# Optimization experiments

Measured on AMD Instinct MI355X. Metric: run time of the kernel, lower is better.

Reference implementation:

```python
import jax, jax.numpy as jnp
import numpy as np

NOT_EPSILON = 1.0
B, Q, K, T = 2, 512, 512, 256  # batch, num queries, num keys, dims


def swishmax(x, axis):
    # x * exp(x - max) / (sum(|x * exp(x - max)|) + 1)
    xexp = x * jnp.exp(x - jnp.max(x, axis=axis, keepdims=True))
    return xexp / (jnp.sum(jnp.abs(xexp), axis=axis, keepdims=True) + NOT_EPSILON)


def setup_inputs() -> dict:
    key = jax.random.key(0)
    ks = jax.random.split(key, 8)
    s = 1.0 / np.sqrt(T)
    return {
        "query_tokens": jax.random.normal(ks[0], (B, Q, T), jnp.float32),
        "key_tokens": jax.random.normal(ks[1], (B, K, T), jnp.float32),
        "value_tokens": jax.random.normal(ks[2], (B, K, T), jnp.float32),
        "Wk": jax.random.normal(ks[3], (T, T), jnp.float32) * s,
        "Wq": jax.random.normal(ks[4], (T, T), jnp.float32) * s,
        "Wva": jax.random.normal(ks[5], (T, T), jnp.float32) * s,
        "Wal": jax.random.normal(ks[6], (T, T), jnp.float32) * s,
        "Wvo": jax.random.normal(ks[7], (T, T), jnp.float32) * s,
    }


def reference(query_tokens, key_tokens, value_tokens, Wk, Wq, Wva, Wal, Wvo):
    # torch nn.Linear: y = x @ W.T (no biases)
    k = jnp.einsum('bkt,ut->bku', key_tokens, Wk)      # [B,K,T]
    q = jnp.einsum('bqt,ut->bqu', query_tokens, Wq)    # [B,Q,T]
    # elementwise outer product over token pairs: [B,K,Q,T]
    raw = k[:, :, None, :] * q[:, None, :, :]
    logits = jnp.einsum('bkqt,ut->bkqu', raw, Wal)     # [B,K,Q,T]
    scale = swishmax(logits, axis=-2)                  # normalize over Q
    v = jnp.einsum('bkt,ut->bku', value_tokens, Wva)   # [B,K,T]
    values_scaled = v[:, :, None, :] * scale           # [B,K,Q,T]
    value_sum = values_scaled.sum(axis=-3)             # sum over K -> [B,Q,T]
    return jnp.einsum('bqt,ut->bqu', value_sum, Wvo)   # [B,Q,T]
```

## Files before the change

### kernel.cpp

```cpp
#include <hip/hip_runtime.h>
#include <cstdint>


typedef short bf16x8 __attribute__((ext_vector_type(8)));
typedef float f32x4  __attribute__((ext_vector_type(4)));

__device__ inline float bf2f(short s) {
  return __uint_as_float(((unsigned)(unsigned short)s) << 16);
}
__device__ inline unsigned packrn(float lo, float hi) {
  return __builtin_amdgcn_perm(__float_as_uint(hi) + 0x8000u,
                               __float_as_uint(lo) + 0x8000u, 0x07060302u);
}
__device__ inline unsigned encM(float f) {
  unsigned k = (unsigned)__float_as_int(f);
  return (k & 0x80000000u) ? ~k : (k | 0x80000000u);
}
__device__ inline float decM(unsigned k) {
  int i = (k & 0x80000000u) ? (int)(k ^ 0x80000000u) : (int)~k;
  return __int_as_float(i);
}

#define FMA16()                                                                 \
  c[0][0] += a.x*w.x; c[0][1] += a.x*w.y; c[0][2] += a.x*w.z; c[0][3] += a.x*w.w; \
  c[1][0] += a.y*w.x; c[1][1] += a.y*w.y; c[1][2] += a.y*w.z; c[1][3] += a.y*w.w; \
  c[2][0] += a.z*w.x; c[2][1] += a.z*w.y; c[2][2] += a.z*w.z; c[2][3] += a.z*w.w; \
  c[3][0] += a.w*w.x; c[3][1] += a.w*w.y; c[3][2] += a.w*w.z; c[3][3] += a.w*w.w;

#define GEMM_BODY_RM(X, W)                                                      \
  __shared__ __align__(16) float As[16][68];                                    \
  __shared__ __align__(16) float Ws[16][68];                                    \
  const int tid = threadIdx.x;                                                  \
  const int tx4 = (tid & 15) * 4;                                               \
  const int ty4 = (tid >> 4) * 4;                                               \
  const int m0 = blockIdx.x * 64, u0 = blockIdx.y * 64;                         \
  const int lmi = tid >> 2, lc4 = (tid & 3) * 4;                                \
  float c[4][4] = {};                                                           \
  _Pragma("unroll 1")                                                           \
  for (int t0 = 0; t0 < 256; t0 += 16) {                                        \
    const float4 xa = *(const float4*)&(X)[(size_t)(m0 + lmi) * 256 + t0 + lc4];\
    const float4 wb = *(const float4*)&(W)[(size_t)(u0 + lmi) * 256 + t0 + lc4];\
    __syncthreads();                                                            \
    As[lc4 + 0][lmi] = xa.x; As[lc4 + 1][lmi] = xa.y;                           \
    As[lc4 + 2][lmi] = xa.z; As[lc4 + 3][lmi] = xa.w;                           \
    Ws[lc4 + 0][lmi] = wb.x; Ws[lc4 + 1][lmi] = wb.y;                           \
    Ws[lc4 + 2][lmi] = wb.z; Ws[lc4 + 3][lmi] = wb.w;                           \
    __syncthreads();                                                            \
    _Pragma("unroll")                                                           \
    for (int t = 0; t < 16; ++t) {                                              \
      const float4 a = *(const float4*)&As[t][ty4];                             \
      const float4 w = *(const float4*)&Ws[t][tx4];                             \
      FMA16();                                                                  \
    }                                                                           \
  }

__global__ __launch_bounds__(256) void proj3(
    const float* __restrict__ key, const float* __restrict__ value,
    const float* __restrict__ query, const float* __restrict__ Wk,
    const float* __restrict__ Wq, const float* __restrict__ Wva,
    const float* __restrict__ Wal, float* __restrict__ kproj,
    float* __restrict__ vproj, short* __restrict__ qpF,
    short* __restrict__ WalF, float* __restrict__ vsum)
{
  const int z = blockIdx.z;
  if (z == 3) {
    const int p = blockIdx.x * 4 + blockIdx.y;
    const int t256 = threadIdx.x;
#pragma unroll
    for (int e = 0; e < 4; ++e) {
      const int d = p * 1024 + t256 * 4 + e;
      const int j = d & 7, uu = (d >> 3) & 31, c8g = d >> 8;
      const int ucx = c8g >> 5, cc = c8g & 31;
      const float v = Wal[(ucx * 32 + uu) * 256 + cc * 8 + j];
      WalF[d] = (short)packrn(v, v);
    }
    float4* vz = (float4*)(vsum + p * 4096);
#pragma unroll
    for (int e = 0; e < 4; ++e) vz[t256 * 4 + e] = make_float4(0.f, 0.f, 0.f, 0.f);
    return;
  }
  const float* X = (z == 0) ? key : (z == 1) ? value : query;
  const float* W = (z == 0) ? Wk  : (z == 1) ? Wva   : Wq;
  GEMM_BODY_RM(X, W);
  if (z == 2) {
    const int tbase = u0 + tx4;
    const int ks = tbase >> 5, l4f = (tbase & 31) >> 3, j0 = tbase & 7;
#pragma unroll
    for (int i = 0; i < 4; ++i) {
      const int m = m0 + ty4 + i;
      const int bb = m >> 9, q = m & 511;
      const int g = q >> 4, l15q = q & 15;
      const size_t idx = ((size_t)(((bb * 32 + g) * 8 + ks) * 64) + l4f * 16 + l15q) * 8 + j0;
      uint2 s; s.x = packrn(c[i][0], c[i][1]); s.y = packrn(c[i][2], c[i][3]);
      *(uint2*)&qpF[idx] = s;
    }
  } else {
    float* C = (z == 0) ? kproj : vproj;
#pragma unroll
    for (int i = 0; i < 4; ++i)
      *(float4*)&C[(size_t)(m0 + ty4 + i) * 256 + u0 + tx4] =
          make_float4(c[i][0], c[i][1], c[i][2], c[i][3]);
  }
}

__global__ __launch_bounds__(256) void gemm_out(
    const float* __restrict__ X, const float* __restrict__ W, float* __restrict__ out)
{
  GEMM_BODY_RM(X, W);
#pragma unroll
  for (int i = 0; i < 4; ++i)
    *(float4*)&out[(size_t)(m0 + ty4 + i) * 256 + u0 + tx4] =
        make_float4(c[i][0], c[i][1], c[i][2], c[i][3]);
}

union Frag { bf16x8 v; unsigned u[4]; };

__global__ __launch_bounds__(1024, 4) void kernelC(
    const short* __restrict__ qpF, const float* __restrict__ kproj,
    const float* __restrict__ vproj, const short* __restrict__ WalF,
    float* __restrict__ vsum)
{
  __shared__ __align__(16) short W2F[2][8192];
  __shared__ float vpS[32 * 33];
  __shared__ unsigned statM[96];
  __shared__ float statS[96];

  const int kt = blockIdx.x, uc = blockIdx.y, b = blockIdx.z;
  const int u0 = uc * 32, k0 = kt * 32;
  const int tid = threadIdx.x;
  const int lane = tid & 63, w = tid >> 6;
  const int l15 = lane & 15, l4 = lane >> 4;
  const int uu = tid & 31, c8 = tid >> 5;

  if (tid < 96) { statM[tid] = 0u; statS[tid] = 0.f; }
  vpS[c8 * 33 + uu] = vproj[(size_t)(b * 512 + k0 + c8) * 256 + u0 + uu];

  float wl[8];
  {
    const bf16x8 w0 = *(const bf16x8*)&WalF[((size_t)(uc * 32 + c8) * 32 + uu) * 8];
#pragma unroll
    for (int j = 0; j < 8; ++j) wl[j] = bf2f(w0[j]);
  }

  const short* qbase = qpF + (size_t)b * 131072;
  Frag qa[2][8];
#pragma unroll
  for (int qg = 0; qg < 2; ++qg)
#pragma unroll
    for (int ks = 0; ks < 8; ++ks) {
      qa[qg][ks].v = *(const bf16x8*)&qbase[(((size_t)(w * 2 + qg) * 8 + ks) * 64 + lane) * 8];
      asm volatile("" : "+v"(qa[qg][ks].u[0]), "+v"(qa[qg][ks].u[1]),
                        "+v"(qa[qg][ks].u[2]), "+v"(qa[qg][ks].u[3]));
    }

  {
    const long krow = (long)(b * 512 + k0) * 256;
    const f32x4 a0 = *(const f32x4*)&kproj[krow + c8 * 8];
    const f32x4 a1 = *(const f32x4*)&kproj[krow + c8 * 8 + 4];
    uint4 st;
    st.x = packrn(wl[0] * a0[0], wl[1] * a0[1]);
    st.y = packrn(wl[2] * a0[2], wl[3] * a0[3]);
    st.z = packrn(wl[4] * a1[0], wl[5] * a1[1]);
    st.w = packrn(wl[6] * a1[2], wl[7] * a1[3]);
    *(uint4*)&W2F[0][(c8 * 32 + uu) * 8] = st;
  }
  __syncthreads();

  const f32x4 z4 = {0.f, 0.f, 0.f, 0.f};
  f32x4 acc[2][2] = {z4, z4, z4, z4};

#pragma unroll 1
  for (int kk = 0; kk < 32; ++kk) {
    const int cs = kk & 1, ss = kk % 3;

    f32x4 a0, a1;
    if (kk < 31) {
      const long krn = (long)(b * 512 + k0 + kk + 1) * 256;
      a0 = *(const f32x4*)&kproj[krn + c8 * 8];
      a1 = *(const f32x4*)&kproj[krn + c8 * 8 + 4];
    }

    f32x4 lg[2][2] = {z4, z4, z4, z4};
#pragma unroll
    for (int ks = 0; ks < 8; ++ks) {
      const bf16x8 f0 = *(const bf16x8*)&W2F[cs][((ks * 4 + l4) * 32 + l15) * 8];
      const bf16x8 f1 = *(const bf16x8*)&W2F[cs][((ks * 4 + l4) * 32 + 16 + l15) * 8];
#pragma unroll
      for (int qg = 0; qg < 2; ++qg) {
        lg[qg][0] = __builtin_amdgcn_mfma_f32_16x16x32_bf16(qa[qg][ks].v, f0, lg[qg][0], 0, 0, 0);
        lg[qg][1] = __builtin_amdgcn_mfma_f32_16x16x32_bf16(qa[qg][ks].v, f1, lg[qg][1], 0, 0, 0);
      }
    }

    if (kk < 31) {
      uint4 st;
      st.x = packrn(wl[0] * a0[0], wl[1] * a0[1]);
      st.y = packrn(wl[2] * a0[2], wl[3] * a0[3]);
      st.z = packrn(wl[4] * a1[0], wl[5] * a1[1]);
      st.w = packrn(wl[6] * a1[2], wl[7] * a1[3]);
      *(uint4*)&W2F[cs ^ 1][(c8 * 32 + uu) * 8] = st;
    }

    float Mv[2], Sv[2];
#pragma unroll
    for (int ug = 0; ug < 2; ++ug) {
      float m = lg[0][ug][0];
#pragma unroll
      for (int qg = 0; qg < 2; ++qg)
#pragma unroll
        for (int i = 0; i < 4; ++i) m = fmaxf(m, lg[qg][ug][i]);
      float s = 0.f;
#pragma unroll
      for (int qg = 0; qg < 2; ++qg)
#pragma unroll
        for (int i = 0; i < 4; ++i) {
          const float x = lg[qg][ug][i];
          const float p = x * __expf(x);
          lg[qg][ug][i] = p;
          s += fabsf(p);
        }
      m = fmaxf(m, __shfl_xor(m, 16));
      m = fmaxf(m, __shfl_xor(m, 32));
      s += __shfl_xor(s, 16);
      s += __shfl_xor(s, 32);
      Mv[ug] = m; Sv[ug] = s;
    }
    if (l4 == 0) {
      atomicMax(&statM[ss * 32 + l15],      encM(Mv[0]));
      atomicMax(&statM[ss * 32 + 16 + l15], encM(Mv[1]));
      atomicAdd(&statS[ss * 32 + l15],      Sv[0]);
      atomicAdd(&statS[ss * 32 + 16 + l15], Sv[1]);
    }
    __syncthreads();

#pragma unroll
    for (int ug = 0; ug < 2; ++ug) {
      const int ui = ug * 16 + l15;
      const float M = decM(statM[ss * 32 + ui]);
      const float S = statS[ss * 32 + ui];
      const float em = __expf(-M);
      const float g = vpS[kk * 33 + ui] * em * __builtin_amdgcn_rcpf(fmaf(S, em, 1.0f));
#pragma unroll
      for (int qg = 0; qg < 2; ++qg)
#pragma unroll
        for (int i = 0; i < 4; ++i)
          acc[qg][ug][i] = fmaf(g, lg[qg][ug][i], acc[qg][ug][i]);
    }
    const int rs = (kk + 2) % 3;
    if (tid < 32) { statM[rs * 32 + tid] = 0u; statS[rs * 32 + tid] = 0.f; }
  }

#pragma unroll
  for (int qg = 0; qg < 2; ++qg)
#pragma unroll
    for (int ug = 0; ug < 2; ++ug)
#pragma unroll
      for (int i = 0; i < 4; ++i)
        atomicAdd(&vsum[(size_t)(b * 512 + w * 32 + qg * 16 + l4 * 4 + i) * 256 +
                        u0 + ug * 16 + l15],
                  acc[qg][ug][i]);
}

extern "C" void kernel_launch(void* const* d_in, const int* in_sizes, int n_in,
                              void* d_out, int out_size, void* d_ws, size_t ws_size,
                              hipStream_t stream) {
  const float* query = (const float*)d_in[0];
  const float* key   = (const float*)d_in[1];
  const float* value = (const float*)d_in[2];
  const float* Wk    = (const float*)d_in[3];
  const float* Wq    = (const float*)d_in[4];
  const float* Wva   = (const float*)d_in[5];
  const float* Wal   = (const float*)d_in[6];
  const float* Wvo   = (const float*)d_in[7];
  float* ws = (float*)d_ws;

  float* kproj = ws;
  float* vproj = kproj + 262144;
  float* vsum  = vproj + 262144;
  short* qpF   = (short*)(vsum + 262144);
  short* WalF  = qpF + 262144;
  float* out   = (float*)d_out;

  proj3<<<dim3(16, 4, 4), 256, 0, stream>>>(key, value, query, Wk, Wq, Wva, Wal,
                                            kproj, vproj, qpF, WalF, vsum);
  kernelC<<<dim3(16, 8, 2), 1024, 0, stream>>>(qpF, kproj, vproj, WalF, vsum);
  gemm_out<<<dim3(16, 4), 256, 0, stream>>>(vsum, Wvo, out);
}
```

Before: 209.2 us.

## Defer swishmax normalization one iteration and interleave logit MFMAs with reductions

Applying the normalized scale to the accumulators is delayed by one key iteration. Each iteration first consumes the previous iteration's block-wide max and sum statistics, which were already synchronized, then computes new logits. The MFMA loop is split per output group, so the max and exp-sum reduction of one group can overlap the MFMAs of the other, and the next W2F tile store moves after the compute. Slot reset in the three-slot statistics ring shifts to match, and an epilogue applies the last iteration. The aim is to hide the barrier and atomic latency behind MFMA work; the cost is higher register pressure from keeping the logits live across iterations.

```diff
diff --git a/kernel.cpp b/kernel.cpp
--- a/kernel.cpp
+++ b/kernel.cpp
@@ -168,6 +168,7 @@
 
   const f32x4 z4 = {0.f, 0.f, 0.f, 0.f};
   f32x4 acc[2][2] = {z4, z4, z4, z4};
+  f32x4 lg[2][2]  = {z4, z4, z4, z4};
 
 #pragma unroll 1
   for (int kk = 0; kk < 32; ++kk) {
@@ -180,30 +181,35 @@
       a1 = *(const f32x4*)&kproj[krn + c8 * 8 + 4];
     }
 
-    f32x4 lg[2][2] = {z4, z4, z4, z4};
-#pragma unroll
-    for (int ks = 0; ks < 8; ++ks) {
-      const bf16x8 f0 = *(const bf16x8*)&W2F[cs][((ks * 4 + l4) * 32 + l15) * 8];
-      const bf16x8 f1 = *(const bf16x8*)&W2F[cs][((ks * 4 + l4) * 32 + 16 + l15) * 8];
-#pragma unroll
-      for (int qg = 0; qg < 2; ++qg) {
-        lg[qg][0] = __builtin_amdgcn_mfma_f32_16x16x32_bf16(qa[qg][ks].v, f0, lg[qg][0], 0, 0, 0);
-        lg[qg][1] = __builtin_amdgcn_mfma_f32_16x16x32_bf16(qa[qg][ks].v, f1, lg[qg][1], 0, 0, 0);
+    if (kk > 0) {
+      const int as = (kk + 2) % 3;
+#pragma unroll
+      for (int ug = 0; ug < 2; ++ug) {
+        const int ui = ug * 16 + l15;
+        const float M = decM(statM[as * 32 + ui]);
+        const float S = statS[as * 32 + ui];
+        const float em = __expf(-M);
+        const float g = vpS[(kk - 1) * 33 + ui] * em *
+                        __builtin_amdgcn_rcpf(fmaf(S, em, 1.0f));
+#pragma unroll
+        for (int qg = 0; qg < 2; ++qg)
+#pragma unroll
+          for (int i = 0; i < 4; ++i)
+            acc[qg][ug][i] = fmaf(g, lg[qg][ug][i], acc[qg][ug][i]);
       }
     }
 
-    if (kk < 31) {
-      uint4 st;
-      st.x = packrn(wl[0] * a0[0], wl[1] * a0[1]);
-      st.y = packrn(wl[2] * a0[2], wl[3] * a0[3]);
-      st.z = packrn(wl[4] * a1[0], wl[5] * a1[1]);
-      st.w = packrn(wl[6] * a1[2], wl[7] * a1[3]);
-      *(uint4*)&W2F[cs ^ 1][(c8 * 32 + uu) * 8] = st;
-    }
-
     float Mv[2], Sv[2];
 #pragma unroll
     for (int ug = 0; ug < 2; ++ug) {
+      lg[0][ug] = z4; lg[1][ug] = z4;
+#pragma unroll
+      for (int ks = 0; ks < 8; ++ks) {
+        const bf16x8 f =
+            *(const bf16x8*)&W2F[cs][((ks * 4 + l4) * 32 + ug * 16 + l15) * 8];
+        lg[0][ug] = __builtin_amdgcn_mfma_f32_16x16x32_bf16(qa[0][ks].v, f, lg[0][ug], 0, 0, 0);
+        lg[1][ug] = __builtin_amdgcn_mfma_f32_16x16x32_bf16(qa[1][ks].v, f, lg[1][ug], 0, 0, 0);
+      }
       float m = lg[0][ug][0];
 #pragma unroll
       for (int qg = 0; qg < 2; ++qg)
@@ -225,29 +231,43 @@
       s += __shfl_xor(s, 32);
       Mv[ug] = m; Sv[ug] = s;
     }
+
+    if (kk < 31) {
+      uint4 st;
+      st.x = packrn(wl[0] * a0[0], wl[1] * a0[1]);
+      st.y = packrn(wl[2] * a0[2], wl[3] * a0[3]);
+      st.z = packrn(wl[4] * a1[0], wl[5] * a1[1]);
+      st.w = packrn(wl[6] * a1[2], wl[7] * a1[3]);
+      *(uint4*)&W2F[cs ^ 1][(c8 * 32 + uu) * 8] = st;
+    }
+
     if (l4 == 0) {
       atomicMax(&statM[ss * 32 + l15],      encM(Mv[0]));
       atomicMax(&statM[ss * 32 + 16 + l15], encM(Mv[1]));
       atomicAdd(&statS[ss * 32 + l15],      Sv[0]);
       atomicAdd(&statS[ss * 32 + 16 + l15], Sv[1]);
     }
+    const int rs = (kk + 1) % 3;
+    if (tid < 32) { statM[rs * 32 + tid] = 0u; statS[rs * 32 + tid] = 0.f; }
     __syncthreads();
-
+  }
+
+  {
+    const int as = 1;
 #pragma unroll
     for (int ug = 0; ug < 2; ++ug) {
       const int ui = ug * 16 + l15;
-      const float M = decM(statM[ss * 32 + ui]);
-      const float S = statS[ss * 32 + ui];
+      const float M = decM(statM[as * 32 + ui]);
+      const float S = statS[as * 32 + ui];
       const float em = __expf(-M);
-      const float g = vpS[kk * 33 + ui] * em * __builtin_amdgcn_rcpf(fmaf(S, em, 1.0f));
+      const float g = vpS[31 * 33 + ui] * em *
+                      __builtin_amdgcn_rcpf(fmaf(S, em, 1.0f));
 #pragma unroll
       for (int qg = 0; qg < 2; ++qg)
 #pragma unroll
         for (int i = 0; i < 4; ++i)
           acc[qg][ug][i] = fmaf(g, lg[qg][ug][i], acc[qg][ug][i]);
     }
-    const int rs = (kk + 2) % 3;
-    if (tid < 32) { statM[rs * 32 + tid] = 0u; statS[rs * 32 + tid] = 0.f; }
   }
 
 #pragma unroll
```

Result: slower. 214.6 us (+2.6%).
